# Kernel tuning notes

Measured on AMD Instinct MI355X. Metric: run time of the kernel, lower is better.

The kernel has to match this reference:

```python
import jax, jax.numpy as jnp
import numpy as np

N_HEADS = 16
HEAD_DIM = 64
WINDOW = 128
GLOBAL = 64


def setup_inputs() -> dict:
    key = jax.random.key(0)
    ks = jax.random.split(key, 5)
    B, T, D = 2, 8192, 1024
    s = 0.02
    return {
        "x": jax.random.normal(ks[0], (B, T, D), dtype=jnp.float32),
        "Wq": jax.random.normal(ks[1], (D, D), dtype=jnp.float32) * s,
        "Wk": jax.random.normal(ks[2], (D, D), dtype=jnp.float32) * s,
        "Wv": jax.random.normal(ks[3], (D, D), dtype=jnp.float32) * s,
        "Wo": jax.random.normal(ks[4], (D, D), dtype=jnp.float32) * s,
    }


def reference(x, Wq, Wk, Wv, Wo):
    B, T, D = x.shape
    h, hd, w = N_HEADS, HEAD_DIM, WINDOW
    g = min(GLOBAL, T)
    nw = T // w  # T chosen as a multiple of window_size
    scale = hd ** -0.5

    def proj(W):
        # nn.Linear: y = x @ W.T ; then (B,T,h,hd) -> (B,h,T,hd)
        return (x @ W.T).reshape(B, T, h, hd).transpose(0, 2, 1, 3)

    q = proj(Wq)
    k = proj(Wk)
    v = proj(Wv)

    # Chunk into non-overlapping local windows: (B,h,nw,w,hd)
    qw = q.reshape(B, h, nw, w, hd)
    kw = k.reshape(B, h, nw, w, hd)
    vw = v.reshape(B, h, nw, w, hd)
    kg = k[:, :, :g, :]  # global prefix keys (B,h,g,hd)
    vg = v[:, :, :g, :]

    # Scores against [global ++ local] keys (faithful: global prefix is
    # concatenated for every window, including windows that overlap it).
    s_g = jnp.einsum("bhnqd,bhgd->bhnqg", qw, kg) * scale  # (B,h,nw,w,g)
    s_l = jnp.einsum("bhnqd,bhnkd->bhnqk", qw, kw) * scale  # (B,h,nw,w,w)
    attn = jax.nn.softmax(jnp.concatenate([s_g, s_l], axis=-1), axis=-1)

    out = (
        jnp.einsum("bhnqg,bhgd->bhnqd", attn[..., :g], vg)
        + jnp.einsum("bhnqk,bhnkd->bhnqd", attn[..., g:], vw)
    )
    out = out.reshape(B, h, T, hd).transpose(0, 2, 1, 3).reshape(B, T, D)
    return out @ Wo.T
```

## Files before the change

kernel.cpp:

```cpp
#include <hip/hip_runtime.h>

typedef unsigned short u16;
typedef __attribute__((ext_vector_type(8))) short short8;
typedef __attribute__((ext_vector_type(4))) float f32x4;
typedef __attribute__((ext_vector_type(16))) float f32x16;
typedef __attribute__((ext_vector_type(4))) float floatx4;
typedef __attribute__((ext_vector_type(4))) unsigned short ushort4v;
typedef __attribute__((ext_vector_type(8))) unsigned short ushort8v;

#define MFMA(a, b, c)   __builtin_amdgcn_mfma_f32_16x16x32_bf16(a, b, c, 0, 0, 0)
#define MFMA32(a, b, c) __builtin_amdgcn_mfma_f32_32x32x16_bf16(a, b, c, 0, 0, 0)

__device__ __forceinline__ u16 f2bf(float f) {
    unsigned u = __float_as_uint(f);
    u += 0x7fffu + ((u >> 16) & 1u);
    return (u16)(u >> 16);
}

__device__ __forceinline__ void async16(const void* g, void* l) {
    __builtin_amdgcn_global_load_lds(
        (const __attribute__((address_space(1))) void*)g,
        (__attribute__((address_space(3))) void*)l, 16, 0, 0);
}

__global__ void cvt_all(const float* __restrict__ x,
                        const float* __restrict__ w0, const float* __restrict__ w1,
                        const float* __restrict__ w2, const float* __restrict__ w3,
                        u16* __restrict__ d, int nx4, int nw4) {
    int total = nx4 + 4 * nw4;
    int i = blockIdx.x * blockDim.x + threadIdx.x;
    int stride = gridDim.x * blockDim.x;
    for (; i < total; i += stride) {
        floatx4 v;
        if (i < nx4) {
            v = ((const floatx4*)x)[i];
        } else {
            int t = i - nx4;
            int w = t >> 18;
            int j = t & (nw4 - 1);
            const float* s = w == 0 ? w0 : (w == 1 ? w1 : (w == 2 ? w2 : w3));
            v = ((const floatx4*)s)[j];
        }
        ushort4v o;
        o[0] = f2bf(v[0]); o[1] = f2bf(v[1]); o[2] = f2bf(v[2]); o[3] = f2bf(v[3]);
        ((ushort4v*)d)[i] = o;
    }
}

template <bool BF16_OUT>
__global__ __launch_bounds__(256) void gemm_nt(
    const u16* __restrict__ A, const u16* __restrict__ B0,
    const u16* __restrict__ B1, const u16* __restrict__ B2,
    void* __restrict__ Cv, int M, int N, int K)
{
    __shared__ u16 As[128 * 64];
    __shared__ u16 Bs[128 * 64];
    const int tid = threadIdx.x;
    const int wave = tid >> 6, lane = tid & 63;
    const int l32 = lane & 31, kh = lane >> 5;
    const int m0 = blockIdx.x * 128, n0 = blockIdx.y * 128;
    const int wm = wave >> 1, wn = wave & 1;
    const u16* Bm = blockIdx.z == 0 ? B0 : (blockIdx.z == 1 ? B1 : B2);
    const size_t coff = (size_t)blockIdx.z * M * N;

    f32x16 acc[2][2];
#pragma unroll
    for (int i = 0; i < 2; i++)
#pragma unroll
        for (int j = 0; j < 2; j++) acc[i][j] = (f32x16)(0.0f);

    const int srow = tid >> 3, sslot = tid & 7;
    const int gch = sslot ^ (srow & 7);
    const u16* ar[4];
    const u16* br[4];
#pragma unroll
    for (int i = 0; i < 4; i++) {
        ar[i] = A  + (size_t)(m0 + i * 32 + srow) * K + gch * 8;
        br[i] = Bm + (size_t)(n0 + i * 32 + srow) * K + gch * 8;
    }

    const int rxor = l32 & 7;

    for (int k0 = 0; k0 < K; k0 += 64) {
#pragma unroll
        for (int i = 0; i < 4; i++) {
            int ldsbase = (i * 256 + wave * 64) * 8;
            async16(ar[i] + k0, (u16*)As + ldsbase);
            async16(br[i] + k0, (u16*)Bs + ldsbase);
        }
        __syncthreads();
#pragma unroll
        for (int kc = 0; kc < 4; kc++) {
            const int rs = ((kc * 2 + kh) ^ rxor) * 8;
            short8 af[2], bg[2];
#pragma unroll
            for (int t = 0; t < 2; t++) {
                af[t] = *(const short8*)&As[(wm * 64 + t * 32 + l32) * 64 + rs];
                bg[t] = *(const short8*)&Bs[(wn * 64 + t * 32 + l32) * 64 + rs];
            }
#pragma unroll
            for (int mt = 0; mt < 2; mt++)
#pragma unroll
                for (int nt = 0; nt < 2; nt++)
                    acc[mt][nt] = MFMA32(af[mt], bg[nt], acc[mt][nt]);
        }
        __syncthreads();
    }

#pragma unroll
    for (int mt = 0; mt < 2; mt++)
#pragma unroll
        for (int nt = 0; nt < 2; nt++)
#pragma unroll
            for (int r = 0; r < 16; r++) {
                int row = m0 + wm * 64 + mt * 32 + 4 * kh + (r & 3) + 8 * (r >> 2);
                int col = n0 + wn * 64 + nt * 32 + l32;
                if constexpr (BF16_OUT)
                    ((u16*)Cv)[coff + (size_t)row * N + col] = f2bf(acc[mt][nt][r]);
                else
                    ((float*)Cv)[coff + (size_t)row * N + col] = acc[mt][nt][r];
            }
}

__global__ __launch_bounds__(256) void attn_win(
    const u16* __restrict__ qkv, u16* __restrict__ outb)
{
    constexpr int T = 8192, D = 1024, HD = 64, G = 64, WIN = 128;
    constexpr int MTOT = 2 * T;
    __shared__ u16 Vt[64 * 200];
    __shared__ u16 KP[12800];

    const int blk = blockIdx.x;
    const int half = blk & 1;
    const int nwin = (blk >> 1) & 63;
    const int h = (blk >> 7) & 15;
    const int b = blk >> 11;
    const int tid = threadIdx.x;
    const int wave = tid >> 6, lane = tid & 63;
    const int quad = lane >> 4, tl = lane & 15;
    const int win0 = nwin * WIN;
    const int q0 = win0 + half * 64;
    const size_t brow = (size_t)b * T;
    const u16* qb = qkv;
    const u16* kb = qkv + (size_t)MTOT * D;
    const u16* vb = qkv + (size_t)2 * MTOT * D;

#pragma unroll
    for (int i = 0; i < 6; i++) {
        int ch = i * 256 + tid;
        int row = ch >> 3, c = ch & 7;
        int tok = row < G ? row : win0 + (row - G);
        async16(vb + (brow + tok) * D + h * HD + c * 8,
                (u16*)KP + (i * 256 + wave * 64) * 8);
    }

    short8 bq[2];
    {
        int tok = q0 + wave * 16 + tl;
        const u16* qrow = qb + (brow + tok) * D + h * HD;
        bq[0] = *(const short8*)(qrow + quad * 8);
        bq[1] = *(const short8*)(qrow + 32 + quad * 8);
    }

    __syncthreads();

    {
        const int d = tid & 63;
#pragma unroll
        for (int i = 0; i < 6; i++) {
            int c = i * 4 + wave;
            ushort8v v;
#pragma unroll
            for (int j = 0; j < 8; j++) v[j] = KP[(c * 8 + j) * 64 + d];
            *(ushort8v*)&Vt[d * 200 + c * 8] = v;
        }
    }

    __syncthreads();

#pragma unroll
    for (int i = 0; i < 6; i++) {
        int ch = i * 256 + tid;
        int row = ch >> 3, slot = ch & 7;
        int g = slot ^ (row & 7);
        int tok = row < G ? row : win0 + (row - G);
        async16(kb + (brow + tok) * D + h * HD + g * 8,
                (u16*)KP + (i * 256 + wave * 64) * 8);
    }

    __syncthreads();

    f32x4 s[12];
#pragma unroll
    for (int kt = 0; kt < 12; kt++) s[kt] = (f32x4)(0.0f);
#pragma unroll
    for (int kt = 0; kt < 12; kt++) {
        int row = kt * 16 + tl;
        int s0 = quad ^ (tl & 7);
        int s1 = (4 + quad) ^ (tl & 7);
        short8 a0 = *(const short8*)&KP[row * 64 + s0 * 8];
        short8 a1 = *(const short8*)&KP[row * 64 + s1 * 8];
        s[kt] = MFMA(a0, bq[0], s[kt]);
        s[kt] = MFMA(a1, bq[1], s[kt]);
    }

    const float c1 = 0.125f * 1.4426950408889634f;
    float mx = -1e30f;
#pragma unroll
    for (int kt = 0; kt < 12; kt++)
#pragma unroll
        for (int r = 0; r < 4; r++) mx = fmaxf(mx, s[kt][r]);
    mx = fmaxf(mx, __shfl_xor(mx, 16, 64));
    mx = fmaxf(mx, __shfl_xor(mx, 32, 64));
    float sum = 0.f;
#pragma unroll
    for (int kt = 0; kt < 12; kt++)
#pragma unroll
        for (int r = 0; r < 4; r++) {
            float e = exp2f((s[kt][r] - mx) * c1);
            s[kt][r] = e;
            sum += e;
        }
    sum += __shfl_xor(sum, 16, 64);
    sum += __shfl_xor(sum, 32, 64);
    float inv = 1.f / sum;

    __syncthreads();

    u16* Pl = (u16*)KP;
    {
        int lq = wave * 16 + tl;
#pragma unroll
        for (int kt = 0; kt < 12; kt++) {
            ushort4v p;
#pragma unroll
            for (int r = 0; r < 4; r++) p[r] = f2bf(s[kt][r] * inv);
            *(ushort4v*)&Pl[lq * 200 + kt * 16 + quad * 4] = p;
        }
    }
    __syncthreads();

    f32x4 o[4];
#pragma unroll
    for (int dt = 0; dt < 4; dt++) o[dt] = (f32x4)(0.0f);
#pragma unroll
    for (int ks = 0; ks < 6; ks++) {
        short8 pa = *(const short8*)&Pl[(wave * 16 + tl) * 200 + ks * 32 + quad * 8];
#pragma unroll
        for (int dt = 0; dt < 4; dt++) {
            short8 vv = *(const short8*)&Vt[(dt * 16 + tl) * 200 + ks * 32 + quad * 8];
            o[dt] = MFMA(pa, vv, o[dt]);
        }
    }

#pragma unroll
    for (int dt = 0; dt < 4; dt++)
#pragma unroll
        for (int r = 0; r < 4; r++) {
            int qq = q0 + wave * 16 + quad * 4 + r;
            int dim = dt * 16 + tl;
            outb[(brow + qq) * D + h * HD + dim] = f2bf(o[dt][r]);
        }
}

extern "C" void kernel_launch(void* const* d_in, const int* in_sizes, int n_in,
                              void* d_out, int out_size, void* d_ws, size_t ws_size,
                              hipStream_t stream)
{
    const float* x  = (const float*)d_in[0];
    const float* Wq = (const float*)d_in[1];
    const float* Wk = (const float*)d_in[2];
    const float* Wv = (const float*)d_in[3];
    const float* Wo = (const float*)d_in[4];

    const int M = 16384, D = 1024;
    u16* xb  = (u16*)d_ws;
    u16* wqb = xb  + (size_t)M * D;
    u16* wob = wqb + (size_t)3 * D * D;
    u16* qkv = wob + (size_t)D * D;
    u16* att = qkv + (size_t)3 * M * D;

    cvt_all<<<2560, 256, 0, stream>>>(x, Wq, Wk, Wv, Wo, xb,
                                      M * D / 4, D * D / 4);

    gemm_nt<true ><<<dim3(M / 128, D / 128, 3), 256, 0, stream>>>(
        xb, wqb, wqb + (size_t)D * D, wqb + (size_t)2 * D * D, qkv, M, D, D);
    attn_win<<<dim3(4096), 256, 0, stream>>>(qkv, att);
    gemm_nt<false><<<dim3(M / 128, D / 128, 1), 256, 0, stream>>>(
        att, wob, wob, wob, d_out, M, D, D);
}
```

Baseline: 337.8 us.

## Rewrite GEMM as 256x256 double-buffered pipeline with 16x16 MFMA and 8 waves

The NT GEMM moves from 128x128 tiles with 4 waves and a single LDS buffer to 256x256 tiles with 8 waves and double-buffered LDS. The next K tile is prefetched in quarters with global-to-LDS loads, interleaved with four MFMA phases, gated by vmcnt waits, barriers and s_setprio. The 32x32 MFMA is replaced by 16x16x32 MFMA. The aim is to hide global load latency and raise data reuse per block, at the cost of 128KB of LDS and fewer blocks in the grid, which may cause tail or occupancy issues.

Result: faster. 305.8 us (-9.5%).

```diff
diff --git a/kernel.cpp b/kernel.cpp
--- a/kernel.cpp
+++ b/kernel.cpp
@@ -3,13 +3,11 @@
 typedef unsigned short u16;
 typedef __attribute__((ext_vector_type(8))) short short8;
 typedef __attribute__((ext_vector_type(4))) float f32x4;
-typedef __attribute__((ext_vector_type(16))) float f32x16;
 typedef __attribute__((ext_vector_type(4))) float floatx4;
 typedef __attribute__((ext_vector_type(4))) unsigned short ushort4v;
 typedef __attribute__((ext_vector_type(8))) unsigned short ushort8v;
 
 #define MFMA(a, b, c)   __builtin_amdgcn_mfma_f32_16x16x32_bf16(a, b, c, 0, 0, 0)
-#define MFMA32(a, b, c) __builtin_amdgcn_mfma_f32_32x32x16_bf16(a, b, c, 0, 0, 0)
 
 __device__ __forceinline__ u16 f2bf(float f) {
     unsigned u = __float_as_uint(f);
@@ -22,6 +20,13 @@
         (const __attribute__((address_space(1))) void*)g,
         (__attribute__((address_space(3))) void*)l, 16, 0, 0);
 }
+
+#define SYNC(n) do {                                             \
+    asm volatile("s_waitcnt vmcnt(" #n ")" ::: "memory");        \
+    __builtin_amdgcn_s_barrier();                                \
+    asm volatile("" ::: "memory");                               \
+    __builtin_amdgcn_sched_barrier(0);                           \
+} while (0)
 
 __global__ void cvt_all(const float* __restrict__ x,
                         const float* __restrict__ w0, const float* __restrict__ w1,
@@ -48,77 +53,144 @@
 }
 
 template <bool BF16_OUT>
-__global__ __launch_bounds__(256) void gemm_nt(
+__global__ __launch_bounds__(512, 2) void gemm_nt(
     const u16* __restrict__ A, const u16* __restrict__ B0,
     const u16* __restrict__ B1, const u16* __restrict__ B2,
     void* __restrict__ Cv, int M, int N, int K)
 {
-    __shared__ u16 As[128 * 64];
-    __shared__ u16 Bs[128 * 64];
+    __shared__ u16 As[2][16384];
+    __shared__ u16 Bs[2][16384];
     const int tid = threadIdx.x;
     const int wave = tid >> 6, lane = tid & 63;
-    const int l32 = lane & 31, kh = lane >> 5;
-    const int m0 = blockIdx.x * 128, n0 = blockIdx.y * 128;
-    const int wm = wave >> 1, wn = wave & 1;
+    const int tl = lane & 15, quad = lane >> 4, xr = lane & 7;
+    const int wm = wave >> 2, wn = wave & 3;
+    const int m0 = blockIdx.x * 256, n0 = blockIdx.y * 256;
     const u16* Bm = blockIdx.z == 0 ? B0 : (blockIdx.z == 1 ? B1 : B2);
     const size_t coff = (size_t)blockIdx.z * M * N;
 
-    f32x16 acc[2][2];
-#pragma unroll
-    for (int i = 0; i < 2; i++)
-#pragma unroll
-        for (int j = 0; j < 2; j++) acc[i][j] = (f32x16)(0.0f);
-
-    const int srow = tid >> 3, sslot = tid & 7;
-    const int gch = sslot ^ (srow & 7);
-    const u16* ar[4];
-    const u16* br[4];
-#pragma unroll
-    for (int i = 0; i < 4; i++) {
-        ar[i] = A  + (size_t)(m0 + i * 32 + srow) * K + gch * 8;
-        br[i] = Bm + (size_t)(n0 + i * 32 + srow) * K + gch * 8;
-    }
-
-    const int rxor = l32 & 7;
-
-    for (int k0 = 0; k0 < K; k0 += 64) {
+    f32x4 acc[8][4];
+#pragma unroll
+    for (int i = 0; i < 8; i++)
+#pragma unroll
+        for (int j = 0; j < 4; j++) acc[i][j] = (f32x4)(0.0f);
+
+    const int rw = lane >> 3, sl = lane & 7;
+    const int g = sl ^ rw;
+    const u16* a_srcb = A  + (size_t)(m0 + wave * 8 + rw) * K + g * 8;
+    const u16* b_srcb = Bm + (size_t)(n0 + (wave >> 2) * 64 + (wave & 3) * 8 + rw) * K + g * 8;
+    u16* asd = &As[0][0] + wave * 512;
+    u16* bsd = &Bs[0][0] + (wave >> 2) * 4096 + (wave & 3) * 512;
+
+#define STG_A(t, h, p) do {                                                              \
+    async16(a_srcb + (size_t)((h) * 64) * K + (size_t)(t) * 64,                          \
+            asd + (p) * 16384 + (h) * 4096);                                             \
+    async16(a_srcb + (size_t)((h) * 64 + 128) * K + (size_t)(t) * 64,                    \
+            asd + (p) * 16384 + (h) * 4096 + 8192);                                      \
+} while (0)
+#define STG_B(t, h, p) do {                                                              \
+    async16(b_srcb + (size_t)((h) * 32) * K + (size_t)(t) * 64,                          \
+            bsd + (p) * 16384 + (h) * 2048);                                             \
+    async16(b_srcb + (size_t)((h) * 32 + 128) * K + (size_t)(t) * 64,                    \
+            bsd + (p) * 16384 + (h) * 2048 + 8192);                                      \
+} while (0)
+
+    const int NT = K >> 6;
+    const u16* Ab0 = &As[0][0] + (wm * 128 + tl) * 64;
+    const u16* Bb0 = &Bs[0][0] + (wn * 64 + tl) * 64;
+    const int s0 = (quad ^ xr) * 8;
+
+    short8 afA[4][2], afB[4][2], bfA[2][2], bfB[2][2];
+
+    STG_A(0, 0, 0); STG_B(0, 0, 0); STG_A(0, 1, 0); STG_B(0, 1, 0);
+
+    for (int t = 0; t < NT; ++t) {
+        const int p = t & 1, pq = p ^ 1;
+        const bool pf = (t + 1) < NT;
+        const u16* Ab = Ab0 + p * 16384;
+        const u16* Bb = Bb0 + p * 16384;
+
+        SYNC(4);
 #pragma unroll
         for (int i = 0; i < 4; i++) {
-            int ldsbase = (i * 256 + wave * 64) * 8;
-            async16(ar[i] + k0, (u16*)As + ldsbase);
-            async16(br[i] + k0, (u16*)Bs + ldsbase);
-        }
-        __syncthreads();
-#pragma unroll
-        for (int kc = 0; kc < 4; kc++) {
-            const int rs = ((kc * 2 + kh) ^ rxor) * 8;
-            short8 af[2], bg[2];
-#pragma unroll
-            for (int t = 0; t < 2; t++) {
-                af[t] = *(const short8*)&As[(wm * 64 + t * 32 + l32) * 64 + rs];
-                bg[t] = *(const short8*)&Bs[(wn * 64 + t * 32 + l32) * 64 + rs];
-            }
-#pragma unroll
-            for (int mt = 0; mt < 2; mt++)
-#pragma unroll
-                for (int nt = 0; nt < 2; nt++)
-                    acc[mt][nt] = MFMA32(af[mt], bg[nt], acc[mt][nt]);
-        }
-        __syncthreads();
-    }
-
-#pragma unroll
-    for (int mt = 0; mt < 2; mt++)
-#pragma unroll
-        for (int nt = 0; nt < 2; nt++)
-#pragma unroll
-            for (int r = 0; r < 16; r++) {
-                int row = m0 + wm * 64 + mt * 32 + 4 * kh + (r & 3) + 8 * (r >> 2);
-                int col = n0 + wn * 64 + nt * 32 + l32;
+            afA[i][0] = *(const short8*)(Ab + i * 1024 + s0);
+            afA[i][1] = *(const short8*)(Ab + i * 1024 + (s0 ^ 32));
+        }
+#pragma unroll
+        for (int j = 0; j < 2; j++) {
+            bfA[j][0] = *(const short8*)(Bb + j * 1024 + s0);
+            bfA[j][1] = *(const short8*)(Bb + j * 1024 + (s0 ^ 32));
+        }
+        if (pf) STG_A(t + 1, 0, pq);
+        __builtin_amdgcn_s_setprio(1);
+#pragma unroll
+        for (int kh = 0; kh < 2; kh++)
+#pragma unroll
+            for (int i = 0; i < 4; i++)
+#pragma unroll
+                for (int j = 0; j < 2; j++)
+                    acc[i][j] = MFMA(afA[i][kh], bfA[j][kh], acc[i][j]);
+        __builtin_amdgcn_s_setprio(0);
+
+        if (pf) { SYNC(4); } else { SYNC(2); }
+#pragma unroll
+        for (int i = 0; i < 4; i++) {
+            afB[i][0] = *(const short8*)(Ab + (4 + i) * 1024 + s0);
+            afB[i][1] = *(const short8*)(Ab + (4 + i) * 1024 + (s0 ^ 32));
+        }
+        if (pf) STG_B(t + 1, 0, pq);
+        __builtin_amdgcn_s_setprio(1);
+#pragma unroll
+        for (int kh = 0; kh < 2; kh++)
+#pragma unroll
+            for (int i = 0; i < 4; i++)
+#pragma unroll
+                for (int j = 0; j < 2; j++)
+                    acc[4 + i][j] = MFMA(afB[i][kh], bfA[j][kh], acc[4 + i][j]);
+        __builtin_amdgcn_s_setprio(0);
+
+        if (pf) { SYNC(4); } else { SYNC(0); }
+#pragma unroll
+        for (int j = 0; j < 2; j++) {
+            bfB[j][0] = *(const short8*)(Bb + (2 + j) * 1024 + s0);
+            bfB[j][1] = *(const short8*)(Bb + (2 + j) * 1024 + (s0 ^ 32));
+        }
+        if (pf) STG_A(t + 1, 1, pq);
+        __builtin_amdgcn_s_setprio(1);
+#pragma unroll
+        for (int kh = 0; kh < 2; kh++)
+#pragma unroll
+            for (int i = 0; i < 4; i++)
+#pragma unroll
+                for (int j = 0; j < 2; j++)
+                    acc[4 + i][2 + j] = MFMA(afB[i][kh], bfB[j][kh], acc[4 + i][2 + j]);
+        __builtin_amdgcn_s_setprio(0);
+
+        if (pf) STG_B(t + 1, 1, pq);
+        __builtin_amdgcn_s_setprio(1);
+#pragma unroll
+        for (int kh = 0; kh < 2; kh++)
+#pragma unroll
+            for (int i = 0; i < 4; i++)
+#pragma unroll
+                for (int j = 0; j < 2; j++)
+                    acc[i][2 + j] = MFMA(afA[i][kh], bfB[j][kh], acc[i][2 + j]);
+        __builtin_amdgcn_s_setprio(0);
+    }
+#undef STG_A
+#undef STG_B
+
+#pragma unroll
+    for (int mf = 0; mf < 8; mf++)
+#pragma unroll
+        for (int nf = 0; nf < 4; nf++)
+#pragma unroll
+            for (int r = 0; r < 4; r++) {
+                int row = m0 + wm * 128 + mf * 16 + quad * 4 + r;
+                int col = n0 + wn * 64 + nf * 16 + tl;
                 if constexpr (BF16_OUT)
-                    ((u16*)Cv)[coff + (size_t)row * N + col] = f2bf(acc[mt][nt][r]);
+                    ((u16*)Cv)[coff + (size_t)row * N + col] = f2bf(acc[mf][nf][r]);
                 else
-                    ((float*)Cv)[coff + (size_t)row * N + col] = acc[mt][nt][r];
+                    ((float*)Cv)[coff + (size_t)row * N + col] = acc[mf][nf][r];
             }
 }
 
@@ -283,9 +355,9 @@
     cvt_all<<<2560, 256, 0, stream>>>(x, Wq, Wk, Wv, Wo, xb,
                                       M * D / 4, D * D / 4);
 
-    gemm_nt<true ><<<dim3(M / 128, D / 128, 3), 256, 0, stream>>>(
+    gemm_nt<true ><<<dim3(M / 256, D / 256, 3), 512, 0, stream>>>(
         xb, wqb, wqb + (size_t)D * D, wqb + (size_t)2 * D * D, qkv, M, D, D);
     attn_win<<<dim3(4096), 256, 0, stream>>>(qkv, att);
-    gemm_nt<false><<<dim3(M / 128, D / 128, 1), 256, 0, stream>>>(
+    gemm_nt<false><<<dim3(M / 256, D / 256, 1), 512, 0, stream>>>(
         att, wob, wob, wob, d_out, M, D, D);
 }
```
